# Kernel optimization log

Hardware: AMD Instinct MI355X
Metric: run time of the kernel (lower is better)

Reference implementation:

```python
import jax, jax.numpy as jnp
import numpy as np

N = 50000
E = 600000
H = 128
LN_EPS = 1e-5


def _layer_norm(h, g, b):
    mu = jnp.mean(h, axis=-1, keepdims=True)
    var = jnp.var(h, axis=-1, keepdims=True)
    return (h - mu) * jax.lax.rsqrt(var + LN_EPS) * g + b


def _mlp(h, params):
    # params = (w0, b0, w1, b1, w2, b2, ln_g, ln_b); mlp_layers=2 pattern:
    # Linear->ReLU->Linear->ReLU->Linear->LayerNorm
    w0, b0, w1, b1, w2, b2, g, be = params
    h = jax.nn.relu(h @ w0 + b0)
    h = jax.nn.relu(h @ w1 + b1)
    h = h @ w2 + b2
    return _layer_norm(h, g, be)


def setup_inputs() -> dict:
    key = jax.random.key(0)
    ks = jax.random.split(key, 16)
    def lin(k, fan_in, fan_out):
        lim = 1.0 / np.sqrt(fan_in)
        kw, kb = jax.random.split(k)
        w = jax.random.uniform(kw, (fan_in, fan_out), jnp.float32, -lim, lim)
        b = jax.random.uniform(kb, (fan_out,), jnp.float32, -lim, lim)
        return w, b
    x = jax.random.normal(ks[0], (N, H), jnp.float32)
    e = jax.random.normal(ks[1], (E, H), jnp.float32)
    edge_index = jax.random.randint(ks[2], (2, E), 0, N, jnp.int64)
    we0, be0 = lin(ks[3], 3 * H, H)
    we1, be1 = lin(ks[4], H, H)
    we2, be2 = lin(ks[5], H, H)
    wn0, bn0 = lin(ks[6], 2 * H, H)
    wn1, bn1 = lin(ks[7], H, H)
    wn2, bn2 = lin(ks[8], H, H)
    return {
        "x": x, "e": e, "edge_index": edge_index,
        "we0": we0, "be0": be0, "we1": we1, "be1": be1, "we2": we2, "be2": be2,
        "ge": jnp.ones((H,), jnp.float32), "bge": jnp.zeros((H,), jnp.float32),
        "wn0": wn0, "bn0": bn0, "wn1": wn1, "bn1": bn1, "wn2": wn2, "bn2": bn2,
        "gn": jnp.ones((H,), jnp.float32), "bgn": jnp.zeros((H,), jnp.float32),
    }


def reference(x, e, edge_index,
              we0, be0, we1, be1, we2, be2, ge, bge,
              wn0, bn0, wn1, bn1, wn2, bn2, gn, bgn):
    src = edge_index[0]
    dst = edge_index[1]
    # gather node feats per edge -> [E, 3H] -> edge MLP -> [E, H]
    edge_in = jnp.concatenate([x[dst], x[src], e], axis=-1)
    e_new = _mlp(edge_in, (we0, be0, we1, be1, we2, be2, ge, bge))
    # scatter-add edge messages into destination nodes -> [N, H]
    agg = jax.ops.segment_sum(e_new, dst, num_segments=x.shape[0])
    node_in = jnp.concatenate([x, agg], axis=-1)
    x_new = x + _mlp(node_in, (wn0, bn0, wn1, bn1, wn2, bn2, gn, bgn))
    return (x_new, e_new)
```

## Files before the change

### kernel.cpp

```cpp
#include <hip/hip_runtime.h>

#define NN 50000
#define NE 600000
#define HD 128

typedef __attribute__((ext_vector_type(8))) short short8;
typedef __attribute__((ext_vector_type(4))) float floatx4;
typedef __attribute__((ext_vector_type(2))) float floatx2;

__device__ __forceinline__ unsigned short f2bf(float f) {
  unsigned int u = __builtin_bit_cast(unsigned int, f);
  u += 0x7FFFu + ((u >> 16) & 1u);
  return (unsigned short)(u >> 16);
}

__device__ __forceinline__ short8 cvt8(const float* __restrict__ p) {
  floatx4 v0 = *(const floatx4*)p;
  floatx4 v1 = *(const floatx4*)(p + 4);
  short8 r;
  r[0] = (short)f2bf(v0[0]); r[1] = (short)f2bf(v0[1]);
  r[2] = (short)f2bf(v0[2]); r[3] = (short)f2bf(v0[3]);
  r[4] = (short)f2bf(v1[0]); r[5] = (short)f2bf(v1[1]);
  r[6] = (short)f2bf(v1[2]); r[7] = (short)f2bf(v1[3]);
  return r;
}

__device__ __forceinline__ void pack_one(const float* __restrict__ w,
                                         unsigned short* __restrict__ wp, int p) {
  int j = p & 7, lane = (p >> 3) & 63, t = p >> 9;
  int n0 = t & 7, k0 = t >> 3;
  int k = k0 * 32 + (lane >> 4) * 8 + j;
  int n = n0 * 16 + (lane & 15);
  wp[p] = f2bf(w[k * HD + n]);
}

__global__ void prep_kernel(const float* __restrict__ we0, const float* __restrict__ we1,
                            const float* __restrict__ we2, const float* __restrict__ wn0,
                            const float* __restrict__ wn1, const float* __restrict__ wn2,
                            unsigned short* __restrict__ wpack,
                            const float* __restrict__ x, unsigned short* __restrict__ xb,
                            int* __restrict__ cnt, int do_cnt, int do_cvt) {
  int p = blockIdx.x * 256 + threadIdx.x;
  if (p < 147456) {
    const float* src;
    int rel;
    if (p < 49152) { src = we0; rel = p; }
    else if (p < 65536) { src = we1; rel = p - 49152; }
    else if (p < 81920) { src = we2; rel = p - 65536; }
    else if (p < 114688) { src = wn0; rel = p - 81920; }
    else if (p < 131072) { src = wn1; rel = p - 114688; }
    else { src = wn2; rel = p - 131072; }
    pack_one(src, wpack + (p - rel), rel);
  } else if (p < 197456) {
    if (do_cnt) cnt[p - 147456] = 0;
  } else if (p < 997456) {
    if (do_cvt) {
      int q = p - 197456;
      *(short8*)(xb + (size_t)q * 8) = cvt8(x + (size_t)q * 8);
    }
  }
}

__global__ void hist_kernel(const int* __restrict__ idx, int* __restrict__ cnt) {
  int eid = blockIdx.x * 256 + threadIdx.x;
  if (eid < NE) atomicAdd(&cnt[idx[NE + eid]], 1);
}

__global__ __launch_bounds__(1024) void scan_kernel(const int* __restrict__ cnt,
                                                    int* __restrict__ offs,
                                                    int* __restrict__ cur) {
  __shared__ int part[1024];
  int t = threadIdx.x;
  int base = t * 49;
  int s = 0;
  for (int i = 0; i < 49; ++i) {
    int g = base + i;
    if (g < NN) s += cnt[g];
  }
  part[t] = s;
  __syncthreads();
  for (int off = 1; off < 1024; off <<= 1) {
    int add = (t >= off) ? part[t - off] : 0;
    __syncthreads();
    part[t] += add;
    __syncthreads();
  }
  int run = part[t] - s;
  for (int i = 0; i < 49; ++i) {
    int g = base + i;
    if (g < NN) {
      int c = cnt[g];
      offs[g] = run;
      cur[g] = run;
      run += c;
    }
  }
  if (t == 1023) offs[NN] = run;
}

__global__ void fill_kernel(const int* __restrict__ idx, int* __restrict__ cur,
                            int* __restrict__ perm) {
  int eid = blockIdx.x * 256 + threadIdx.x;
  if (eid < NE) {
    int d = idx[NE + eid];
    int pos = atomicAdd(&cur[d], 1);
    perm[pos] = eid;
  }
}

template <int KSTEPS>
__device__ __forceinline__ void gemm_tile(const unsigned short* a_base, int a_stride,
                                          const unsigned short* __restrict__ wp,
                                          int lane, floatx4* acc) {
  int quad = lane >> 4, l16 = lane & 15;
  for (int k0 = 0; k0 < KSTEPS; ++k0) {
    short8 a = *(const short8*)(a_base + l16 * a_stride + k0 * 32 + quad * 8);
    const unsigned short* w = wp + k0 * 4096 + lane * 8;
#pragma unroll
    for (int n0 = 0; n0 < 8; ++n0) {
      short8 b = *(const short8*)(w + n0 * 512);
      acc[n0] = __builtin_amdgcn_mfma_f32_16x16x32_bf16(a, b, acc[n0], 0, 0, 0);
    }
  }
}

__device__ __forceinline__ void store_relu_bf16(const floatx4* acc,
                                                const float* __restrict__ bias,
                                                unsigned short* out_base, int stride,
                                                int lane) {
  int quad = lane >> 4, l16 = lane & 15;
#pragma unroll
  for (int n0 = 0; n0 < 8; ++n0) {
    float bv = bias[n0 * 16 + l16];
#pragma unroll
    for (int r = 0; r < 4; ++r) {
      float v = acc[n0][r] + bv;
      v = v > 0.f ? v : 0.f;
      out_base[(quad * 4 + r) * stride + n0 * 16 + l16] = f2bf(v);
    }
  }
}

#define SH 136

template <int XBF, int ATOM>
__global__ __launch_bounds__(256, 4) void edge_kernel(
    const float* __restrict__ x, const unsigned short* __restrict__ xb,
    const float* __restrict__ e, const int* __restrict__ idx,
    const unsigned short* __restrict__ w0p, const float* __restrict__ b0,
    const unsigned short* __restrict__ w1p, const float* __restrict__ b1,
    const unsigned short* __restrict__ w2p, const float* __restrict__ b2,
    const float* __restrict__ g, const float* __restrict__ bg,
    float* __restrict__ e_out, float* __restrict__ agg) {
  __shared__ __align__(16) unsigned short lh[64 * SH];

  int wave = threadIdx.x >> 6, lane = threadIdx.x & 63;
  int quad = lane >> 4, l16 = lane & 15;
  int ebase = blockIdx.x * 64 + wave * 16;
  int arow = ebase + l16;
  int s = idx[arow], d = idx[NE + arow];

  floatx4 acc[8];
  floatx4 z = {0.f, 0.f, 0.f, 0.f};
#pragma unroll
  for (int t = 0; t < 8; ++t) acc[t] = z;

  const float* ee = e + (size_t)arow * HD + quad * 8;
  if constexpr (XBF) {
    const unsigned short* xd = xb + (size_t)d * HD + quad * 8;
    const unsigned short* xs = xb + (size_t)s * HD + quad * 8;
#pragma unroll
    for (int k0 = 0; k0 < 12; ++k0) {
      short8 a;
      if (k0 < 4)
        a = *(const short8*)(xd + k0 * 32);
      else if (k0 < 8)
        a = *(const short8*)(xs + (k0 - 4) * 32);
      else
        a = cvt8(ee + (k0 - 8) * 32);
      const unsigned short* w = w0p + k0 * 4096 + lane * 8;
#pragma unroll
      for (int n0 = 0; n0 < 8; ++n0) {
        short8 b = *(const short8*)(w + n0 * 512);
        acc[n0] = __builtin_amdgcn_mfma_f32_16x16x32_bf16(a, b, acc[n0], 0, 0, 0);
      }
    }
  } else {
    const float* xd = x + (size_t)d * HD + quad * 8;
    const float* xs = x + (size_t)s * HD + quad * 8;
#pragma unroll
    for (int k0 = 0; k0 < 12; ++k0) {
      short8 a;
      if (k0 < 4)
        a = cvt8(xd + k0 * 32);
      else if (k0 < 8)
        a = cvt8(xs + (k0 - 4) * 32);
      else
        a = cvt8(ee + (k0 - 8) * 32);
      const unsigned short* w = w0p + k0 * 4096 + lane * 8;
#pragma unroll
      for (int n0 = 0; n0 < 8; ++n0) {
        short8 b = *(const short8*)(w + n0 * 512);
        acc[n0] = __builtin_amdgcn_mfma_f32_16x16x32_bf16(a, b, acc[n0], 0, 0, 0);
      }
    }
  }
  unsigned short* lhw = lh + wave * 16 * SH;
  store_relu_bf16(acc, b0, lhw, SH, lane);

#pragma unroll
  for (int t = 0; t < 8; ++t) acc[t] = z;
  gemm_tile<4>(lhw, SH, w1p, lane, acc);
  store_relu_bf16(acc, b1, lhw, SH, lane);

#pragma unroll
  for (int t = 0; t < 8; ++t) acc[t] = z;
  gemm_tile<4>(lhw, SH, w2p, lane, acc);

  float h3[8][4];
#pragma unroll
  for (int n0 = 0; n0 < 8; ++n0) {
    float bv = b2[n0 * 16 + l16];
#pragma unroll
    for (int r = 0; r < 4; ++r) h3[n0][r] = acc[n0][r] + bv;
  }
  float s1[4] = {0.f, 0.f, 0.f, 0.f}, s2[4] = {0.f, 0.f, 0.f, 0.f};
#pragma unroll
  for (int n0 = 0; n0 < 8; ++n0)
#pragma unroll
    for (int r = 0; r < 4; ++r) {
      s1[r] += h3[n0][r];
      s2[r] += h3[n0][r] * h3[n0][r];
    }
#pragma unroll
  for (int m = 1; m < 16; m <<= 1) {
#pragma unroll
    for (int r = 0; r < 4; ++r) {
      s1[r] += __shfl_xor(s1[r], m, 64);
      s2[r] += __shfl_xor(s2[r], m, 64);
    }
  }
  float mu[4], rs[4];
#pragma unroll
  for (int r = 0; r < 4; ++r) {
    mu[r] = s1[r] * (1.f / 128.f);
    float var = s2[r] * (1.f / 128.f) - mu[r] * mu[r];
    rs[r] = rsqrtf(var + 1e-5f);
  }
#pragma unroll
  for (int n0 = 0; n0 < 8; ++n0) {
    int col = n0 * 16 + l16;
    float gv = g[col], bv = bg[col];
#pragma unroll
    for (int r = 0; r < 4; ++r) {
      int ei = ebase + quad * 4 + r;
      float v = (h3[n0][r] - mu[r]) * rs[r] * gv + bv;
      e_out[(size_t)ei * HD + col] = v;
      if constexpr (ATOM) {
        int drow = idx[NE + ei];
        atomicAdd(&agg[(size_t)drow * HD + col], v);
      }
    }
  }
}

template <int XBF>
__global__ __launch_bounds__(256, 4) void node_kernel_csr(
    const float* __restrict__ x, const unsigned short* __restrict__ xb,
    const float* __restrict__ e_out, const int* __restrict__ offs,
    const int* __restrict__ perm, const unsigned short* __restrict__ w0p,
    const float* __restrict__ b0, const unsigned short* __restrict__ w1p,
    const float* __restrict__ b1, const unsigned short* __restrict__ w2p,
    const float* __restrict__ b2, const float* __restrict__ g,
    const float* __restrict__ bg, float* __restrict__ x_out) {
  __shared__ __align__(16) unsigned short lh[64 * SH];
  __shared__ __align__(16) unsigned short sag[64 * SH];

  int wave = threadIdx.x >> 6, lane = threadIdx.x & 63;
  int quad = lane >> 4, l16 = lane & 15;
  int nbase = blockIdx.x * 64 + wave * 16;

  unsigned short* sagw = sag + wave * 16 * SH;
  int c0 = lane * 2;
  for (int rr = 0; rr < 16; ++rr) {
    int n = nbase + rr;
    float a0 = 0.f, a1 = 0.f;
    if (n < NN) {
      int beg = offs[n], end = offs[n + 1];
      int j = beg;
      for (; j + 4 <= end; j += 4) {
        int e0 = perm[j], e1 = perm[j + 1], e2 = perm[j + 2], e3 = perm[j + 3];
        floatx2 v0 = *(const floatx2*)(e_out + (size_t)e0 * HD + c0);
        floatx2 v1 = *(const floatx2*)(e_out + (size_t)e1 * HD + c0);
        floatx2 v2 = *(const floatx2*)(e_out + (size_t)e2 * HD + c0);
        floatx2 v3 = *(const floatx2*)(e_out + (size_t)e3 * HD + c0);
        a0 += v0[0] + v1[0] + v2[0] + v3[0];
        a1 += v0[1] + v1[1] + v2[1] + v3[1];
      }
      for (; j < end; ++j) {
        int eid = perm[j];
        floatx2 v = *(const floatx2*)(e_out + (size_t)eid * HD + c0);
        a0 += v[0];
        a1 += v[1];
      }
    }
    unsigned int pk = (unsigned int)f2bf(a0) | ((unsigned int)f2bf(a1) << 16);
    *(unsigned int*)(sagw + rr * SH + c0) = pk;
  }

  int arow = nbase + l16;
  int nc = arow < NN ? arow : NN - 1;

  floatx4 acc[8];
  floatx4 z = {0.f, 0.f, 0.f, 0.f};
#pragma unroll
  for (int t = 0; t < 8; ++t) acc[t] = z;

#pragma unroll
  for (int k0 = 0; k0 < 8; ++k0) {
    short8 a;
    if (k0 < 4) {
      if constexpr (XBF)
        a = *(const short8*)(xb + (size_t)nc * HD + quad * 8 + k0 * 32);
      else
        a = cvt8(x + (size_t)nc * HD + quad * 8 + k0 * 32);
    } else {
      a = *(const short8*)(sagw + l16 * SH + (k0 - 4) * 32 + quad * 8);
    }
    const unsigned short* w = w0p + k0 * 4096 + lane * 8;
#pragma unroll
    for (int n0 = 0; n0 < 8; ++n0) {
      short8 b = *(const short8*)(w + n0 * 512);
      acc[n0] = __builtin_amdgcn_mfma_f32_16x16x32_bf16(a, b, acc[n0], 0, 0, 0);
    }
  }
  unsigned short* lhw = lh + wave * 16 * SH;
  store_relu_bf16(acc, b0, lhw, SH, lane);

#pragma unroll
  for (int t = 0; t < 8; ++t) acc[t] = z;
  gemm_tile<4>(lhw, SH, w1p, lane, acc);
  store_relu_bf16(acc, b1, lhw, SH, lane);

#pragma unroll
  for (int t = 0; t < 8; ++t) acc[t] = z;
  gemm_tile<4>(lhw, SH, w2p, lane, acc);

  float h3[8][4];
#pragma unroll
  for (int n0 = 0; n0 < 8; ++n0) {
    float bv = b2[n0 * 16 + l16];
#pragma unroll
    for (int r = 0; r < 4; ++r) h3[n0][r] = acc[n0][r] + bv;
  }
  float s1[4] = {0.f, 0.f, 0.f, 0.f}, s2[4] = {0.f, 0.f, 0.f, 0.f};
#pragma unroll
  for (int n0 = 0; n0 < 8; ++n0)
#pragma unroll
    for (int r = 0; r < 4; ++r) {
      s1[r] += h3[n0][r];
      s2[r] += h3[n0][r] * h3[n0][r];
    }
#pragma unroll
  for (int m = 1; m < 16; m <<= 1) {
#pragma unroll
    for (int r = 0; r < 4; ++r) {
      s1[r] += __shfl_xor(s1[r], m, 64);
      s2[r] += __shfl_xor(s2[r], m, 64);
    }
  }
  float mu[4], rs[4];
#pragma unroll
  for (int r = 0; r < 4; ++r) {
    mu[r] = s1[r] * (1.f / 128.f);
    float var = s2[r] * (1.f / 128.f) - mu[r] * mu[r];
    rs[r] = rsqrtf(var + 1e-5f);
  }
#pragma unroll
  for (int n0 = 0; n0 < 8; ++n0) {
    int col = n0 * 16 + l16;
    float gv = g[col], bv = bg[col];
#pragma unroll
    for (int r = 0; r < 4; ++r) {
      int ni = nbase + quad * 4 + r;
      if (ni < NN) {
        float v = (h3[n0][r] - mu[r]) * rs[r] * gv + bv;
        x_out[(size_t)ni * HD + col] = x[(size_t)ni * HD + col] + v;
      }
    }
  }
}

template <int XBF>
__global__ __launch_bounds__(256, 4) void node_kernel_atom(
    const float* __restrict__ x, const unsigned short* __restrict__ xb,
    const float* __restrict__ agg, const unsigned short* __restrict__ w0p,
    const float* __restrict__ b0, const unsigned short* __restrict__ w1p,
    const float* __restrict__ b1, const unsigned short* __restrict__ w2p,
    const float* __restrict__ b2, const float* __restrict__ g,
    const float* __restrict__ bg, float* __restrict__ x_out) {
  __shared__ __align__(16) unsigned short lh[64 * SH];

  int wave = threadIdx.x >> 6, lane = threadIdx.x & 63;
  int quad = lane >> 4, l16 = lane & 15;
  int nbase = blockIdx.x * 64 + wave * 16;
  int arow = nbase + l16;
  int nc = arow < NN ? arow : NN - 1;

  floatx4 acc[8];
  floatx4 z = {0.f, 0.f, 0.f, 0.f};
#pragma unroll
  for (int t = 0; t < 8; ++t) acc[t] = z;

  const float* ar = agg + (size_t)nc * HD + quad * 8;
#pragma unroll
  for (int k0 = 0; k0 < 8; ++k0) {
    short8 a;
    if (k0 < 4) {
      if constexpr (XBF)
        a = *(const short8*)(xb + (size_t)nc * HD + quad * 8 + k0 * 32);
      else
        a = cvt8(x + (size_t)nc * HD + quad * 8 + k0 * 32);
    } else {
      a = cvt8(ar + (k0 - 4) * 32);
    }
    const unsigned short* w = w0p + k0 * 4096 + lane * 8;
#pragma unroll
    for (int n0 = 0; n0 < 8; ++n0) {
      short8 b = *(const short8*)(w + n0 * 512);
      acc[n0] = __builtin_amdgcn_mfma_f32_16x16x32_bf16(a, b, acc[n0], 0, 0, 0);
    }
  }
  unsigned short* lhw = lh + wave * 16 * SH;
  store_relu_bf16(acc, b0, lhw, SH, lane);

#pragma unroll
  for (int t = 0; t < 8; ++t) acc[t] = z;
  gemm_tile<4>(lhw, SH, w1p, lane, acc);
  store_relu_bf16(acc, b1, lhw, SH, lane);

#pragma unroll
  for (int t = 0; t < 8; ++t) acc[t] = z;
  gemm_tile<4>(lhw, SH, w2p, lane, acc);

  float h3[8][4];
#pragma unroll
  for (int n0 = 0; n0 < 8; ++n0) {
    float bv = b2[n0 * 16 + l16];
#pragma unroll
    for (int r = 0; r < 4; ++r) h3[n0][r] = acc[n0][r] + bv;
  }
  float s1[4] = {0.f, 0.f, 0.f, 0.f}, s2[4] = {0.f, 0.f, 0.f, 0.f};
#pragma unroll
  for (int n0 = 0; n0 < 8; ++n0)
#pragma unroll
    for (int r = 0; r < 4; ++r) {
      s1[r] += h3[n0][r];
      s2[r] += h3[n0][r] * h3[n0][r];
    }
#pragma unroll
  for (int m = 1; m < 16; m <<= 1) {
#pragma unroll
    for (int r = 0; r < 4; ++r) {
      s1[r] += __shfl_xor(s1[r], m, 64);
      s2[r] += __shfl_xor(s2[r], m, 64);
    }
  }
  float mu[4], rs[4];
#pragma unroll
  for (int r = 0; r < 4; ++r) {
    mu[r] = s1[r] * (1.f / 128.f);
    float var = s2[r] * (1.f / 128.f) - mu[r] * mu[r];
    rs[r] = rsqrtf(var + 1e-5f);
  }
#pragma unroll
  for (int n0 = 0; n0 < 8; ++n0) {
    int col = n0 * 16 + l16;
    float gv = g[col], bv = bg[col];
#pragma unroll
    for (int r = 0; r < 4; ++r) {
      int ni = nbase + quad * 4 + r;
      if (ni < NN) {
        float v = (h3[n0][r] - mu[r]) * rs[r] * gv + bv;
        x_out[(size_t)ni * HD + col] = x[(size_t)ni * HD + col] + v;
      }
    }
  }
}

extern "C" void kernel_launch(void* const* d_in, const int* in_sizes, int n_in,
                              void* d_out, int out_size, void* d_ws, size_t ws_size,
                              hipStream_t stream) {
  const float* x = (const float*)d_in[0];
  const float* e = (const float*)d_in[1];
  const int* idx = (const int*)d_in[2];
  const float* we0 = (const float*)d_in[3];
  const float* be0 = (const float*)d_in[4];
  const float* we1 = (const float*)d_in[5];
  const float* be1 = (const float*)d_in[6];
  const float* we2 = (const float*)d_in[7];
  const float* be2 = (const float*)d_in[8];
  const float* ge = (const float*)d_in[9];
  const float* bge = (const float*)d_in[10];
  const float* wn0 = (const float*)d_in[11];
  const float* bn0 = (const float*)d_in[12];
  const float* wn1 = (const float*)d_in[13];
  const float* bn1 = (const float*)d_in[14];
  const float* wn2 = (const float*)d_in[15];
  const float* bn2 = (const float*)d_in[16];
  const float* gn = (const float*)d_in[17];
  const float* bgn = (const float*)d_in[18];

  float* xout = (float*)d_out;
  float* eout = (float*)d_out + (size_t)NN * HD;

  const size_t WPK = 147456;
  const size_t XBN = (size_t)NN * HD;
  const size_t CSRI = (size_t)NN + (NN + 1) + NN + NE;
  const size_t WB = WPK * 2, XB = XBN * 2, CSRB = CSRI * 4;

  unsigned short* wpack = (unsigned short*)d_ws;
  unsigned short* w0p = wpack;
  unsigned short* w1p = wpack + 49152;
  unsigned short* w2p = wpack + 65536;
  unsigned short* wn0p = wpack + 81920;
  unsigned short* wn1p = wpack + 114688;
  unsigned short* wn2p = wpack + 131072;

  bool use_csr_xb = ws_size >= WB + XB + CSRB;
  bool use_csr = use_csr_xb || ws_size >= WB + CSRB;
  bool use_xb = use_csr_xb || (!use_csr && ws_size >= WB + XB);

  unsigned short* xbuf = wpack + WPK;
  int* ibase = use_xb ? (int*)(wpack + WPK + XBN) : (int*)(wpack + WPK);
  int* cnt = ibase;
  int* offs = cnt + NN;
  int* cur = offs + NN + 1;
  int* perm = cur + NN;

  prep_kernel<<<(997456 + 255) / 256, 256, 0, stream>>>(
      we0, we1, we2, wn0, wn1, wn2, wpack, x, xbuf, cnt, use_csr ? 1 : 0,
      use_xb ? 1 : 0);

  if (use_csr) {
    hist_kernel<<<(NE + 255) / 256, 256, 0, stream>>>(idx, cnt);
    scan_kernel<<<1, 1024, 0, stream>>>(cnt, offs, cur);
    fill_kernel<<<(NE + 255) / 256, 256, 0, stream>>>(idx, cur, perm);
    if (use_xb) {
      edge_kernel<1, 0><<<NE / 64, 256, 0, stream>>>(
          x, xbuf, e, idx, w0p, be0, w1p, be1, w2p, be2, ge, bge, eout, nullptr);
      node_kernel_csr<1><<<(NN + 63) / 64, 256, 0, stream>>>(
          x, xbuf, eout, offs, perm, wn0p, bn0, wn1p, bn1, wn2p, bn2, gn, bgn, xout);
    } else {
      edge_kernel<0, 0><<<NE / 64, 256, 0, stream>>>(
          x, xbuf, e, idx, w0p, be0, w1p, be1, w2p, be2, ge, bge, eout, nullptr);
      node_kernel_csr<0><<<(NN + 63) / 64, 256, 0, stream>>>(
          x, xbuf, eout, offs, perm, wn0p, bn0, wn1p, bn1, wn2p, bn2, gn, bgn, xout);
    }
  } else {
    hipMemsetAsync(xout, 0, (size_t)NN * HD * sizeof(float), stream);
    if (use_xb) {
      edge_kernel<1, 1><<<NE / 64, 256, 0, stream>>>(
          x, xbuf, e, idx, w0p, be0, w1p, be1, w2p, be2, ge, bge, eout, xout);
      node_kernel_atom<1><<<(NN + 63) / 64, 256, 0, stream>>>(
          x, xbuf, xout, wn0p, bn0, wn1p, bn1, wn2p, bn2, gn, bgn, xout);
    } else {
      edge_kernel<0, 1><<<NE / 64, 256, 0, stream>>>(
          x, xbuf, e, idx, w0p, be0, w1p, be1, w2p, be2, ge, bge, eout, xout);
      node_kernel_atom<0><<<(NN + 63) / 64, 256, 0, stream>>>(
          x, xbuf, xout, wn0p, bn0, wn1p, bn1, wn2p, bn2, gn, bgn, xout);
    }
  }
}
```

Baseline: 1.114 ms.

## Stage MLP weights through double-buffered LDS and vectorize CSR gather

Every wave used to read packed bf16 weight slices straight from global memory. Now all three GEMMs in the edge and node kernels run as one loop over 4096-element weight slices. Each slice is prefetched into registers and written to a double-buffered LDS area, with a __syncthreads per step. The CSR aggregation in the node kernel now reads 8 floats per lane across 4 rows per quad instead of 2 floats across 16 rows. This adds 16KB of LDS and per-step block barriers, and the node kernel's launch bounds drop to 3 blocks per CU, which may reduce occupancy.

```diff
diff --git a/kernel.cpp b/kernel.cpp
--- a/kernel.cpp
+++ b/kernel.cpp
@@ -6,7 +6,6 @@
 
 typedef __attribute__((ext_vector_type(8))) short short8;
 typedef __attribute__((ext_vector_type(4))) float floatx4;
-typedef __attribute__((ext_vector_type(2))) float floatx2;
 
 __device__ __forceinline__ unsigned short f2bf(float f) {
   unsigned int u = __builtin_bit_cast(unsigned int, f);
@@ -108,22 +107,6 @@
   }
 }
 
-template <int KSTEPS>
-__device__ __forceinline__ void gemm_tile(const unsigned short* a_base, int a_stride,
-                                          const unsigned short* __restrict__ wp,
-                                          int lane, floatx4* acc) {
-  int quad = lane >> 4, l16 = lane & 15;
-  for (int k0 = 0; k0 < KSTEPS; ++k0) {
-    short8 a = *(const short8*)(a_base + l16 * a_stride + k0 * 32 + quad * 8);
-    const unsigned short* w = wp + k0 * 4096 + lane * 8;
-#pragma unroll
-    for (int n0 = 0; n0 < 8; ++n0) {
-      short8 b = *(const short8*)(w + n0 * 512);
-      acc[n0] = __builtin_amdgcn_mfma_f32_16x16x32_bf16(a, b, acc[n0], 0, 0, 0);
-    }
-  }
-}
-
 __device__ __forceinline__ void store_relu_bf16(const floatx4* acc,
                                                 const float* __restrict__ bias,
                                                 unsigned short* out_base, int stride,
@@ -147,75 +130,85 @@
 __global__ __launch_bounds__(256, 4) void edge_kernel(
     const float* __restrict__ x, const unsigned short* __restrict__ xb,
     const float* __restrict__ e, const int* __restrict__ idx,
-    const unsigned short* __restrict__ w0p, const float* __restrict__ b0,
-    const unsigned short* __restrict__ w1p, const float* __restrict__ b1,
-    const unsigned short* __restrict__ w2p, const float* __restrict__ b2,
-    const float* __restrict__ g, const float* __restrict__ bg,
-    float* __restrict__ e_out, float* __restrict__ agg) {
+    const unsigned short* __restrict__ wall,
+    const float* __restrict__ b0, const float* __restrict__ b1,
+    const float* __restrict__ b2, const float* __restrict__ g,
+    const float* __restrict__ bg, float* __restrict__ e_out,
+    float* __restrict__ agg) {
   __shared__ __align__(16) unsigned short lh[64 * SH];
-
-  int wave = threadIdx.x >> 6, lane = threadIdx.x & 63;
+  __shared__ __align__(16) unsigned short wbuf[2][4096];
+
+  int tid = threadIdx.x;
+  int wave = tid >> 6, lane = tid & 63;
   int quad = lane >> 4, l16 = lane & 15;
   int ebase = blockIdx.x * 64 + wave * 16;
   int arow = ebase + l16;
-  int s = idx[arow], d = idx[NE + arow];
+  int se = idx[arow], de = idx[NE + arow];
+
+  short8 p0 = *(const short8*)(wall + tid * 16);
+  short8 p1 = *(const short8*)(wall + tid * 16 + 8);
+  *(short8*)(&wbuf[0][tid * 16]) = p0;
+  *(short8*)(&wbuf[0][tid * 16 + 8]) = p1;
+
+  const float* ee = e + (size_t)arow * HD + quad * 8;
+  const unsigned short* xd16 = nullptr;
+  const unsigned short* xs16 = nullptr;
+  const float* xdf = nullptr;
+  const float* xsf = nullptr;
+  if constexpr (XBF) {
+    xd16 = xb + (size_t)de * HD + quad * 8;
+    xs16 = xb + (size_t)se * HD + quad * 8;
+  } else {
+    xdf = x + (size_t)de * HD + quad * 8;
+    xsf = x + (size_t)se * HD + quad * 8;
+  }
+  unsigned short* lhw = lh + wave * 16 * SH;
 
   floatx4 acc[8];
   floatx4 z = {0.f, 0.f, 0.f, 0.f};
 #pragma unroll
   for (int t = 0; t < 8; ++t) acc[t] = z;
 
-  const float* ee = e + (size_t)arow * HD + quad * 8;
-  if constexpr (XBF) {
-    const unsigned short* xd = xb + (size_t)d * HD + quad * 8;
-    const unsigned short* xs = xb + (size_t)s * HD + quad * 8;
-#pragma unroll
-    for (int k0 = 0; k0 < 12; ++k0) {
-      short8 a;
-      if (k0 < 4)
-        a = *(const short8*)(xd + k0 * 32);
-      else if (k0 < 8)
-        a = *(const short8*)(xs + (k0 - 4) * 32);
-      else
-        a = cvt8(ee + (k0 - 8) * 32);
-      const unsigned short* w = w0p + k0 * 4096 + lane * 8;
-#pragma unroll
-      for (int n0 = 0; n0 < 8; ++n0) {
-        short8 b = *(const short8*)(w + n0 * 512);
-        acc[n0] = __builtin_amdgcn_mfma_f32_16x16x32_bf16(a, b, acc[n0], 0, 0, 0);
-      }
-    }
-  } else {
-    const float* xd = x + (size_t)d * HD + quad * 8;
-    const float* xs = x + (size_t)s * HD + quad * 8;
-#pragma unroll
-    for (int k0 = 0; k0 < 12; ++k0) {
-      short8 a;
-      if (k0 < 4)
-        a = cvt8(xd + k0 * 32);
-      else if (k0 < 8)
-        a = cvt8(xs + (k0 - 4) * 32);
-      else
-        a = cvt8(ee + (k0 - 8) * 32);
-      const unsigned short* w = w0p + k0 * 4096 + lane * 8;
-#pragma unroll
-      for (int n0 = 0; n0 < 8; ++n0) {
-        short8 b = *(const short8*)(w + n0 * 512);
-        acc[n0] = __builtin_amdgcn_mfma_f32_16x16x32_bf16(a, b, acc[n0], 0, 0, 0);
-      }
-    }
-  }
-  unsigned short* lhw = lh + wave * 16 * SH;
-  store_relu_bf16(acc, b0, lhw, SH, lane);
-
-#pragma unroll
-  for (int t = 0; t < 8; ++t) acc[t] = z;
-  gemm_tile<4>(lhw, SH, w1p, lane, acc);
-  store_relu_bf16(acc, b1, lhw, SH, lane);
-
-#pragma unroll
-  for (int t = 0; t < 8; ++t) acc[t] = z;
-  gemm_tile<4>(lhw, SH, w2p, lane, acc);
+  for (int s = 0; s < 20; ++s) {
+    __syncthreads();
+    if (s < 19) {
+      p0 = *(const short8*)(wall + (s + 1) * 4096 + tid * 16);
+      p1 = *(const short8*)(wall + (s + 1) * 4096 + tid * 16 + 8);
+    }
+    short8 a;
+    if (s < 4) {
+      if constexpr (XBF) a = *(const short8*)(xd16 + s * 32);
+      else a = cvt8(xdf + s * 32);
+    } else if (s < 8) {
+      if constexpr (XBF) a = *(const short8*)(xs16 + (s - 4) * 32);
+      else a = cvt8(xsf + (s - 4) * 32);
+    } else if (s < 12) {
+      a = cvt8(ee + (s - 8) * 32);
+    } else if (s < 16) {
+      a = *(const short8*)(lhw + l16 * SH + (s - 12) * 32 + quad * 8);
+    } else {
+      a = *(const short8*)(lhw + l16 * SH + (s - 16) * 32 + quad * 8);
+    }
+    const unsigned short* wsl = &wbuf[s & 1][0];
+#pragma unroll
+    for (int n0 = 0; n0 < 8; ++n0) {
+      short8 b = *(const short8*)(wsl + n0 * 512 + lane * 8);
+      acc[n0] = __builtin_amdgcn_mfma_f32_16x16x32_bf16(a, b, acc[n0], 0, 0, 0);
+    }
+    if (s == 11) {
+      store_relu_bf16(acc, b0, lhw, SH, lane);
+#pragma unroll
+      for (int t = 0; t < 8; ++t) acc[t] = z;
+    } else if (s == 15) {
+      store_relu_bf16(acc, b1, lhw, SH, lane);
+#pragma unroll
+      for (int t = 0; t < 8; ++t) acc[t] = z;
+    }
+    if (s < 19) {
+      *(short8*)(&wbuf[(s + 1) & 1][tid * 16]) = p0;
+      *(short8*)(&wbuf[(s + 1) & 1][tid * 16 + 8]) = p1;
+    }
+  }
 
   float h3[8][4];
 #pragma unroll
@@ -265,86 +258,115 @@
 }
 
 template <int XBF>
-__global__ __launch_bounds__(256, 4) void node_kernel_csr(
+__global__ __launch_bounds__(256, 3) void node_kernel_csr(
     const float* __restrict__ x, const unsigned short* __restrict__ xb,
     const float* __restrict__ e_out, const int* __restrict__ offs,
-    const int* __restrict__ perm, const unsigned short* __restrict__ w0p,
-    const float* __restrict__ b0, const unsigned short* __restrict__ w1p,
-    const float* __restrict__ b1, const unsigned short* __restrict__ w2p,
+    const int* __restrict__ perm,
+    const unsigned short* __restrict__ wall,
+    const float* __restrict__ b0, const float* __restrict__ b1,
     const float* __restrict__ b2, const float* __restrict__ g,
     const float* __restrict__ bg, float* __restrict__ x_out) {
   __shared__ __align__(16) unsigned short lh[64 * SH];
   __shared__ __align__(16) unsigned short sag[64 * SH];
-
-  int wave = threadIdx.x >> 6, lane = threadIdx.x & 63;
+  __shared__ __align__(16) unsigned short wbuf[2][4096];
+
+  int tid = threadIdx.x;
+  int wave = tid >> 6, lane = tid & 63;
   int quad = lane >> 4, l16 = lane & 15;
   int nbase = blockIdx.x * 64 + wave * 16;
 
+  short8 p0 = *(const short8*)(wall + tid * 16);
+  short8 p1 = *(const short8*)(wall + tid * 16 + 8);
+
   unsigned short* sagw = sag + wave * 16 * SH;
-  int c0 = lane * 2;
-  for (int rr = 0; rr < 16; ++rr) {
-    int n = nbase + rr;
-    float a0 = 0.f, a1 = 0.f;
+  for (int rr = 0; rr < 4; ++rr) {
+    int rloc = quad * 4 + rr;
+    int n = nbase + rloc;
+    float a0 = 0.f, a1 = 0.f, a2 = 0.f, a3 = 0.f;
+    float a4 = 0.f, a5 = 0.f, a6 = 0.f, a7 = 0.f;
     if (n < NN) {
       int beg = offs[n], end = offs[n + 1];
       int j = beg;
-      for (; j + 4 <= end; j += 4) {
-        int e0 = perm[j], e1 = perm[j + 1], e2 = perm[j + 2], e3 = perm[j + 3];
-        floatx2 v0 = *(const floatx2*)(e_out + (size_t)e0 * HD + c0);
-        floatx2 v1 = *(const floatx2*)(e_out + (size_t)e1 * HD + c0);
-        floatx2 v2 = *(const floatx2*)(e_out + (size_t)e2 * HD + c0);
-        floatx2 v3 = *(const floatx2*)(e_out + (size_t)e3 * HD + c0);
-        a0 += v0[0] + v1[0] + v2[0] + v3[0];
-        a1 += v0[1] + v1[1] + v2[1] + v3[1];
+      for (; j + 2 <= end; j += 2) {
+        int e0 = perm[j], e1 = perm[j + 1];
+        const float* r0 = e_out + (size_t)e0 * HD + l16 * 8;
+        const float* r1 = e_out + (size_t)e1 * HD + l16 * 8;
+        floatx4 u0 = *(const floatx4*)r0, u1 = *(const floatx4*)(r0 + 4);
+        floatx4 w0 = *(const floatx4*)r1, w1 = *(const floatx4*)(r1 + 4);
+        a0 += u0[0] + w0[0]; a1 += u0[1] + w0[1];
+        a2 += u0[2] + w0[2]; a3 += u0[3] + w0[3];
+        a4 += u1[0] + w1[0]; a5 += u1[1] + w1[1];
+        a6 += u1[2] + w1[2]; a7 += u1[3] + w1[3];
       }
-      for (; j < end; ++j) {
-        int eid = perm[j];
-        floatx2 v = *(const floatx2*)(e_out + (size_t)eid * HD + c0);
-        a0 += v[0];
-        a1 += v[1];
+      if (j < end) {
+        int e0 = perm[j];
+        const float* r0 = e_out + (size_t)e0 * HD + l16 * 8;
+        floatx4 u0 = *(const floatx4*)r0, u1 = *(const floatx4*)(r0 + 4);
+        a0 += u0[0]; a1 += u0[1]; a2 += u0[2]; a3 += u0[3];
+        a4 += u1[0]; a5 += u1[1]; a6 += u1[2]; a7 += u1[3];
       }
     }
-    unsigned int pk = (unsigned int)f2bf(a0) | ((unsigned int)f2bf(a1) << 16);
-    *(unsigned int*)(sagw + rr * SH + c0) = pk;
-  }
+    short8 pk;
+    pk[0] = (short)f2bf(a0); pk[1] = (short)f2bf(a1);
+    pk[2] = (short)f2bf(a2); pk[3] = (short)f2bf(a3);
+    pk[4] = (short)f2bf(a4); pk[5] = (short)f2bf(a5);
+    pk[6] = (short)f2bf(a6); pk[7] = (short)f2bf(a7);
+    *(short8*)(sagw + rloc * SH + l16 * 8) = pk;
+  }
+
+  *(short8*)(&wbuf[0][tid * 16]) = p0;
+  *(short8*)(&wbuf[0][tid * 16 + 8]) = p1;
 
   int arow = nbase + l16;
   int nc = arow < NN ? arow : NN - 1;
+  const unsigned short* xr16 = nullptr;
+  const float* xrf = nullptr;
+  if constexpr (XBF) xr16 = xb + (size_t)nc * HD + quad * 8;
+  else xrf = x + (size_t)nc * HD + quad * 8;
+  unsigned short* lhw = lh + wave * 16 * SH;
 
   floatx4 acc[8];
   floatx4 z = {0.f, 0.f, 0.f, 0.f};
 #pragma unroll
   for (int t = 0; t < 8; ++t) acc[t] = z;
 
-#pragma unroll
-  for (int k0 = 0; k0 < 8; ++k0) {
+  for (int s = 0; s < 16; ++s) {
+    __syncthreads();
+    if (s < 15) {
+      p0 = *(const short8*)(wall + (s + 1) * 4096 + tid * 16);
+      p1 = *(const short8*)(wall + (s + 1) * 4096 + tid * 16 + 8);
+    }
     short8 a;
-    if (k0 < 4) {
-      if constexpr (XBF)
-        a = *(const short8*)(xb + (size_t)nc * HD + quad * 8 + k0 * 32);
-      else
-        a = cvt8(x + (size_t)nc * HD + quad * 8 + k0 * 32);
+    if (s < 4) {
+      if constexpr (XBF) a = *(const short8*)(xr16 + s * 32);
+      else a = cvt8(xrf + s * 32);
+    } else if (s < 8) {
+      a = *(const short8*)(sagw + l16 * SH + (s - 4) * 32 + quad * 8);
+    } else if (s < 12) {
+      a = *(const short8*)(lhw + l16 * SH + (s - 8) * 32 + quad * 8);
     } else {
-      a = *(const short8*)(sagw + l16 * SH + (k0 - 4) * 32 + quad * 8);
-    }
-    const unsigned short* w = w0p + k0 * 4096 + lane * 8;
+      a = *(const short8*)(lhw + l16 * SH + (s - 12) * 32 + quad * 8);
+    }
+    const unsigned short* wsl = &wbuf[s & 1][0];
 #pragma unroll
     for (int n0 = 0; n0 < 8; ++n0) {
-      short8 b = *(const short8*)(w + n0 * 512);
+      short8 b = *(const short8*)(wsl + n0 * 512 + lane * 8);
       acc[n0] = __builtin_amdgcn_mfma_f32_16x16x32_bf16(a, b, acc[n0], 0, 0, 0);
     }
-  }
-  unsigned short* lhw = lh + wave * 16 * SH;
-  store_relu_bf16(acc, b0, lhw, SH, lane);
-
-#pragma unroll
-  for (int t = 0; t < 8; ++t) acc[t] = z;
-  gemm_tile<4>(lhw, SH, w1p, lane, acc);
-  store_relu_bf16(acc, b1, lhw, SH, lane);
-
-#pragma unroll
-  for (int t = 0; t < 8; ++t) acc[t] = z;
-  gemm_tile<4>(lhw, SH, w2p, lane, acc);
+    if (s == 7) {
+      store_relu_bf16(acc, b0, lhw, SH, lane);
+#pragma unroll
+      for (int t = 0; t < 8; ++t) acc[t] = z;
+    } else if (s == 11) {
+      store_relu_bf16(acc, b1, lhw, SH, lane);
+#pragma unroll
+      for (int t = 0; t < 8; ++t) acc[t] = z;
+    }
+    if (s < 15) {
+      *(short8*)(&wbuf[(s + 1) & 1][tid * 16]) = p0;
+      *(short8*)(&wbuf[(s + 1) & 1][tid * 16 + 8]) = p1;
+    }
+  }
 
   float h3[8][4];
 #pragma unroll
@@ -392,56 +414,77 @@
 }
 
 template <int XBF>
-__global__ __launch_bounds__(256, 4) void node_kernel_atom(
+__global__ __launch_bounds__(256, 4) void node_kernel_agg(
     const float* __restrict__ x, const unsigned short* __restrict__ xb,
-    const float* __restrict__ agg, const unsigned short* __restrict__ w0p,
-    const float* __restrict__ b0, const unsigned short* __restrict__ w1p,
-    const float* __restrict__ b1, const unsigned short* __restrict__ w2p,
+    const float* __restrict__ agg,
+    const unsigned short* __restrict__ wall,
+    const float* __restrict__ b0, const float* __restrict__ b1,
     const float* __restrict__ b2, const float* __restrict__ g,
     const float* __restrict__ bg, float* __restrict__ x_out) {
   __shared__ __align__(16) unsigned short lh[64 * SH];
-
-  int wave = threadIdx.x >> 6, lane = threadIdx.x & 63;
+  __shared__ __align__(16) unsigned short wbuf[2][4096];
+
+  int tid = threadIdx.x;
+  int wave = tid >> 6, lane = tid & 63;
   int quad = lane >> 4, l16 = lane & 15;
   int nbase = blockIdx.x * 64 + wave * 16;
   int arow = nbase + l16;
   int nc = arow < NN ? arow : NN - 1;
 
+  short8 p0 = *(const short8*)(wall + tid * 16);
+  short8 p1 = *(const short8*)(wall + tid * 16 + 8);
+  *(short8*)(&wbuf[0][tid * 16]) = p0;
+  *(short8*)(&wbuf[0][tid * 16 + 8]) = p1;
+
+  const float* ar = agg + (size_t)nc * HD + quad * 8;
+  const unsigned short* xr16 = nullptr;
+  const float* xrf = nullptr;
+  if constexpr (XBF) xr16 = xb + (size_t)nc * HD + quad * 8;
+  else xrf = x + (size_t)nc * HD + quad * 8;
+  unsigned short* lhw = lh + wave * 16 * SH;
+
   floatx4 acc[8];
   floatx4 z = {0.f, 0.f, 0.f, 0.f};
 #pragma unroll
   for (int t = 0; t < 8; ++t) acc[t] = z;
 
-  const float* ar = agg + (size_t)nc * HD + quad * 8;
-#pragma unroll
-  for (int k0 = 0; k0 < 8; ++k0) {
+  for (int s = 0; s < 16; ++s) {
+    __syncthreads();
+    if (s < 15) {
+      p0 = *(const short8*)(wall + (s + 1) * 4096 + tid * 16);
+      p1 = *(const short8*)(wall + (s + 1) * 4096 + tid * 16 + 8);
+    }
     short8 a;
-    if (k0 < 4) {
-      if constexpr (XBF)
-        a = *(const short8*)(xb + (size_t)nc * HD + quad * 8 + k0 * 32);
-      else
-        a = cvt8(x + (size_t)nc * HD + quad * 8 + k0 * 32);
+    if (s < 4) {
+      if constexpr (XBF) a = *(const short8*)(xr16 + s * 32);
+      else a = cvt8(xrf + s * 32);
+    } else if (s < 8) {
+      a = cvt8(ar + (s - 4) * 32);
+    } else if (s < 12) {
+      a = *(const short8*)(lhw + l16 * SH + (s - 8) * 32 + quad * 8);
     } else {
-      a = cvt8(ar + (k0 - 4) * 32);
-    }
-    const unsigned short* w = w0p + k0 * 4096 + lane * 8;
+      a = *(const short8*)(lhw + l16 * SH + (s - 12) * 32 + quad * 8);
+    }
+    const unsigned short* wsl = &wbuf[s & 1][0];
 #pragma unroll
     for (int n0 = 0; n0 < 8; ++n0) {
-      short8 b = *(const short8*)(w + n0 * 512);
+      short8 b = *(const short8*)(wsl + n0 * 512 + lane * 8);
       acc[n0] = __builtin_amdgcn_mfma_f32_16x16x32_bf16(a, b, acc[n0], 0, 0, 0);
     }
-  }
-  unsigned short* lhw = lh + wave * 16 * SH;
-  store_relu_bf16(acc, b0, lhw, SH, lane);
-
-#pragma unroll
-  for (int t = 0; t < 8; ++t) acc[t] = z;
-  gemm_tile<4>(lhw, SH, w1p, lane, acc);
-  store_relu_bf16(acc, b1, lhw, SH, lane);
-
-#pragma unroll
-  for (int t = 0; t < 8; ++t) acc[t] = z;
-  gemm_tile<4>(lhw, SH, w2p, lane, acc);
+    if (s == 7) {
+      store_relu_bf16(acc, b0, lhw, SH, lane);
+#pragma unroll
+      for (int t = 0; t < 8; ++t) acc[t] = z;
+    } else if (s == 11) {
+      store_relu_bf16(acc, b1, lhw, SH, lane);
+#pragma unroll
+      for (int t = 0; t < 8; ++t) acc[t] = z;
+    }
+    if (s < 15) {
+      *(short8*)(&wbuf[(s + 1) & 1][tid * 16]) = p0;
+      *(short8*)(&wbuf[(s + 1) & 1][tid * 16 + 8]) = p1;
+    }
+  }
 
   float h3[8][4];
 #pragma unroll
@@ -520,19 +563,15 @@
   const size_t WB = WPK * 2, XB = XBN * 2, CSRB = CSRI * 4;
 
   unsigned short* wpack = (unsigned short*)d_ws;
-  unsigned short* w0p = wpack;
-  unsigned short* w1p = wpack + 49152;
-  unsigned short* w2p = wpack + 65536;
-  unsigned short* wn0p = wpack + 81920;
-  unsigned short* wn1p = wpack + 114688;
-  unsigned short* wn2p = wpack + 131072;
-
-  bool use_csr_xb = ws_size >= WB + XB + CSRB;
-  bool use_csr = use_csr_xb || ws_size >= WB + CSRB;
-  bool use_xb = use_csr_xb || (!use_csr && ws_size >= WB + XB);
+  const unsigned short* wedge = wpack;
+  const unsigned short* wnode = wpack + 81920;
+
+  bool full = ws_size >= WB + XB + CSRB;
+  bool use_csr = full || ws_size >= WB + CSRB;
+  bool use_xb = full || (!use_csr && ws_size >= WB + XB);
 
   unsigned short* xbuf = wpack + WPK;
-  int* ibase = use_xb ? (int*)(wpack + WPK + XBN) : (int*)(wpack + WPK);
+  int* ibase = (int*)(wpack + WPK + (use_xb ? XBN : 0));
   int* cnt = ibase;
   int* offs = cnt + NN;
   int* cur = offs + NN + 1;
@@ -546,29 +585,29 @@
     hist_kernel<<<(NE + 255) / 256, 256, 0, stream>>>(idx, cnt);
     scan_kernel<<<1, 1024, 0, stream>>>(cnt, offs, cur);
     fill_kernel<<<(NE + 255) / 256, 256, 0, stream>>>(idx, cur, perm);
-    if (use_xb) {
+    if (full) {
       edge_kernel<1, 0><<<NE / 64, 256, 0, stream>>>(
-          x, xbuf, e, idx, w0p, be0, w1p, be1, w2p, be2, ge, bge, eout, nullptr);
+          x, xbuf, e, idx, wedge, be0, be1, be2, ge, bge, eout, nullptr);
       node_kernel_csr<1><<<(NN + 63) / 64, 256, 0, stream>>>(
-          x, xbuf, eout, offs, perm, wn0p, bn0, wn1p, bn1, wn2p, bn2, gn, bgn, xout);
+          x, xbuf, eout, offs, perm, wnode, bn0, bn1, bn2, gn, bgn, xout);
     } else {
       edge_kernel<0, 0><<<NE / 64, 256, 0, stream>>>(
-          x, xbuf, e, idx, w0p, be0, w1p, be1, w2p, be2, ge, bge, eout, nullptr);
+          x, xbuf, e, idx, wedge, be0, be1, be2, ge, bge, eout, nullptr);
       node_kernel_csr<0><<<(NN + 63) / 64, 256, 0, stream>>>(
-          x, xbuf, eout, offs, perm, wn0p, bn0, wn1p, bn1, wn2p, bn2, gn, bgn, xout);
+          x, xbuf, eout, offs, perm, wnode, bn0, bn1, bn2, gn, bgn, xout);
     }
   } else {
     hipMemsetAsync(xout, 0, (size_t)NN * HD * sizeof(float), stream);
     if (use_xb) {
       edge_kernel<1, 1><<<NE / 64, 256, 0, stream>>>(
-          x, xbuf, e, idx, w0p, be0, w1p, be1, w2p, be2, ge, bge, eout, xout);
-      node_kernel_atom<1><<<(NN + 63) / 64, 256, 0, stream>>>(
-          x, xbuf, xout, wn0p, bn0, wn1p, bn1, wn2p, bn2, gn, bgn, xout);
+          x, xbuf, e, idx, wedge, be0, be1, be2, ge, bge, eout, xout);
+      node_kernel_agg<1><<<(NN + 63) / 64, 256, 0, stream>>>(
+          x, xbuf, xout, wnode, bn0, bn1, bn2, gn, bgn, xout);
     } else {
       edge_kernel<0, 1><<<NE / 64, 256, 0, stream>>>(
-          x, xbuf, e, idx, w0p, be0, w1p, be1, w2p, be2, ge, bge, eout, xout);
-      node_kernel_atom<0><<<(NN + 63) / 64, 256, 0, stream>>>(
-          x, xbuf, xout, wn0p, bn0, wn1p, bn1, wn2p, bn2, gn, bgn, xout);
-    }
-  }
-}
+          x, xbuf, e, idx, wedge, be0, be1, be2, ge, bge, eout, xout);
+      node_kernel_agg<0><<<(NN + 63) / 64, 256, 0, stream>>>(
+          x, xbuf, xout, wnode, bn0, bn1, bn2, gn, bgn, xout);
+    }
+  }
+}
```

Result: faster. 1.012 ms (-9.2%).
